# Kernel optimization log

Hardware: AMD Instinct MI355X
Metric: run time of the kernel (lower is better)

## Reference

```python
import jax, jax.numpy as jnp
import numpy as np

VOCAB, EMBED, HIDDEN, CLASSES = 32000, 256, 512, 4
BATCH, SEQ = 64, 512


def setup_inputs() -> dict:
    key = jax.random.key(0)
    ks = jax.random.split(key, 12)
    gd = EMBED + HIDDEN
    s_g = 1.0 / np.sqrt(gd)
    s_f = 1.0 / np.sqrt(HIDDEN)
    return {
        "input_ids": jax.random.randint(ks[0], (BATCH, SEQ), 0, VOCAB, dtype=jnp.int32),
        "embedding": jax.random.normal(ks[1], (VOCAB, EMBED), dtype=jnp.float32),
        "W_f": jax.random.uniform(ks[2], (HIDDEN, gd), jnp.float32, -s_g, s_g),
        "b_f": jax.random.uniform(ks[3], (HIDDEN,), jnp.float32, -s_g, s_g),
        "W_i": jax.random.uniform(ks[4], (HIDDEN, gd), jnp.float32, -s_g, s_g),
        "b_i": jax.random.uniform(ks[5], (HIDDEN,), jnp.float32, -s_g, s_g),
        "W_o": jax.random.uniform(ks[6], (HIDDEN, gd), jnp.float32, -s_g, s_g),
        "b_o": jax.random.uniform(ks[7], (HIDDEN,), jnp.float32, -s_g, s_g),
        "W_c": jax.random.uniform(ks[8], (HIDDEN, gd), jnp.float32, -s_g, s_g),
        "b_c": jax.random.uniform(ks[9], (HIDDEN,), jnp.float32, -s_g, s_g),
        "fc_w": jax.random.uniform(ks[10], (CLASSES, HIDDEN), jnp.float32, -s_f, s_f),
        "fc_b": jax.random.uniform(ks[11], (CLASSES,), jnp.float32, -s_f, s_f),
    }


def reference(input_ids, embedding, W_f, b_f, W_i, b_i, W_o, b_o, W_c, b_c, fc_w, fc_b):
    x = embedding[input_ids]                      # [B, T, E]
    B = x.shape[0]
    xs = jnp.swapaxes(x, 0, 1)                    # [T, B, E]

    def step(carry, x_t):
        h, c = carry
        inp = jnp.concatenate([h, x_t], axis=1)   # [B, H+E]
        f = jax.nn.sigmoid(inp @ W_f.T + b_f)
        i = jax.nn.sigmoid(inp @ W_i.T + b_i)
        o = jax.nn.sigmoid(inp @ W_o.T + b_o)
        g = jnp.tanh(inp @ W_c.T + b_c)
        c_new = f * c + i * g
        h_new = o * jnp.tanh(c_new)
        return (h_new, c_new), h_new

    h0 = jnp.zeros((B, HIDDEN), dtype=x.dtype)
    c0 = jnp.zeros((B, HIDDEN), dtype=x.dtype)
    _, hids = jax.lax.scan(step, (h0, c0), xs)    # hids: [T, B, H]
    max_hids = jnp.max(hids, axis=0)              # [B, H]
    logits = max_hids @ fc_w.T + fc_b             # [B, C]
    return logits
```

## Files before the change

kernel.cpp:

```cpp
#include <hip/hip_runtime.h>
#include <math.h>


#define BATCH   64
#define SEQ     512
#define EMBED   256
#define HIDDEN  512
#define GD      768
#define CLASSES 4

#define NBLK    256
#define NTHR    512
#define GROUPS  4
#define GB      64
#define CPG     16
#define UPB     8
#define ROWS    32

#define SHS  520
#define SXS  264
#define PRS  68

typedef unsigned long long __attribute__((may_alias)) ull_a;

union F2U { float f[2]; unsigned long long u; };

__device__ __forceinline__ float dpp8_sum(float v) {
  int x;
  x = __builtin_amdgcn_update_dpp(0, __float_as_int(v), 0x141, 0xF, 0xF, false);
  v += __int_as_float(x);
  x = __builtin_amdgcn_update_dpp(0, __float_as_int(v), 0x4E,  0xF, 0xF, false);
  v += __int_as_float(x);
  x = __builtin_amdgcn_update_dpp(0, __float_as_int(v), 0xB1,  0xF, 0xF, false);
  v += __int_as_float(x);
  return v;
}

__global__ __launch_bounds__(NTHR) void lstm_persistent(
    const int*   __restrict__ ids,
    const float* __restrict__ emb,
    const float* __restrict__ Wf, const float* __restrict__ bf,
    const float* __restrict__ Wi, const float* __restrict__ bi,
    const float* __restrict__ Wo, const float* __restrict__ bo,
    const float* __restrict__ Wc, const float* __restrict__ bc,
    const float* __restrict__ fcw,
    const float* __restrict__ fcb,
    float* __restrict__ out,
    float* __restrict__ ws)
{
  __shared__ __align__(16) float sH[CPG * SHS];
  __shared__ __align__(16) float sX[CPG * SXS];
  __shared__ __align__(16) float sPart[64 * PRS];
  __shared__ float sG[ROWS][CPG];
  __shared__ float sC[UPB][CPG];
  __shared__ float sM[UPB][CPG];
  __shared__ float sB[ROWS];

  const int tid = threadIdx.x;
  const int bid = blockIdx.x;
  const int g   = bid & 3;
  const int j   = bid >> 2;
  const int u0  = j * UPB;

  float*    hbufF   = ws;
  ull_a*    hbufU   = (ull_a*)ws;
  float*    wmaxF   = ws + (size_t)2 * BATCH * HIDDEN;
  ull_a*    wmaxU   = (ull_a*)wmaxF;
  unsigned* flags   = (unsigned*)(ws + (size_t)3 * BATCH * HIDDEN);
  unsigned* myflag  = flags + (g * 64 + j) * 16;

  const int sl = tid & 7;
  const int wv = tid >> 6;
  const int s  = sl + wv * 8;
  const int rg = (tid >> 3) & 7;

  float4 wh[4][2], wx4[4];
  {
    const float* Wg = (rg < 2) ? Wf : (rg < 4) ? Wi : (rg < 6) ? Wo : Wc;
    const int ub = u0 + (rg & 1) * 4;
    #pragma unroll
    for (int ri = 0; ri < 4; ++ri) {
      const float* row = Wg + (size_t)(ub + ri) * GD;
      wh[ri][0] = *(const float4*)(row + s * 8);
      wh[ri][1] = *(const float4*)(row + s * 8 + 4);
      wx4[ri]   = *(const float4*)(row + HIDDEN + s * 4);
    }
  }
  if (tid < ROWS) {
    const float* bv = (tid < 8) ? bf : (tid < 16) ? bi : (tid < 24) ? bo : bc;
    sB[tid] = bv[u0 + (tid & 7)];
  }
  if (tid < UPB * CPG) {
    ((float*)sC)[tid] = 0.0f;
    ((float*)sM)[tid] = -3.402823e38f;
  }

  const int stg_c = tid >> 5;
  const int stg_s = tid & 31;
  const int bStg  = g * CPG + stg_c;

  const float* pH = sH + s * 8;
  const float* pX = sX + s * 4;

  float4 rx0, rx1;
  {
    int id0 = ids[(size_t)bStg * SEQ];
    const float4* xs = (const float4*)(emb + (size_t)id0 * EMBED);
    rx0 = xs[stg_s * 2];
    rx1 = xs[stg_s * 2 + 1];
  }

  for (int t = 0; t < SEQ; ++t) {
    const int pb = t & 1;

    {
      float* dx = sX + stg_c * SXS + stg_s * 8;
      *(float4*)dx = rx0;
      *(float4*)(dx + 4) = rx1;
    }

    if (tid < 64) {
      const unsigned* pf = flags + (g * 64 + tid) * 16;
      while (true) {
        unsigned v = __hip_atomic_load(pf, __ATOMIC_RELAXED,
                                       __HIP_MEMORY_SCOPE_AGENT);
        if (__all((int)(v >= (unsigned)t))) break;
        __builtin_amdgcn_s_sleep(1);
      }
    }
    __atomic_signal_fence(__ATOMIC_ACQUIRE);
    __syncthreads();

    {
      const ull_a* hs = hbufU + ((size_t)pb * BATCH + bStg) * (HIDDEN / 2);
      float* dh = sH + stg_c * SHS;
      #pragma unroll
      for (int kk = 0; kk < 8; ++kk) {
        unsigned long long v = __hip_atomic_load(hs + stg_s + kk * 32,
                                                 __ATOMIC_RELAXED,
                                                 __HIP_MEMORY_SCOPE_AGENT);
        *(ull_a*)(dh + 2 * stg_s + 64 * kk) = v;
      }
    }
    __syncthreads();

    #pragma unroll
    for (int ci = 0; ci < 16; ++ci) {
      float4 xv = *(const float4*)(pX + ci * SXS);
      float4 h0 = *(const float4*)(pH + ci * SHS);
      float4 h1 = *(const float4*)(pH + ci * SHS + 4);
      float a[4];
      #pragma unroll
      for (int ri = 0; ri < 4; ++ri) {
        float t0;
        t0 = wx4[ri].x * xv.x;
        t0 = fmaf(wx4[ri].y, xv.y, t0);
        t0 = fmaf(wx4[ri].z, xv.z, t0);
        t0 = fmaf(wx4[ri].w, xv.w, t0);
        t0 = fmaf(wh[ri][0].x, h0.x, t0);
        t0 = fmaf(wh[ri][0].y, h0.y, t0);
        t0 = fmaf(wh[ri][0].z, h0.z, t0);
        t0 = fmaf(wh[ri][0].w, h0.w, t0);
        t0 = fmaf(wh[ri][1].x, h1.x, t0);
        t0 = fmaf(wh[ri][1].y, h1.y, t0);
        t0 = fmaf(wh[ri][1].z, h1.z, t0);
        t0 = fmaf(wh[ri][1].w, h1.w, t0);
        a[ri] = dpp8_sum(t0);
      }
      if ((tid & 7) == 0) {
        float* dst = sPart + (tid >> 3) * PRS + ci;
        dst[0]  = a[0];
        dst[16] = a[1];
        dst[32] = a[2];
        dst[48] = a[3];
      }
    }

    {
      const int tn = (t + 1 < SEQ) ? t + 1 : SEQ - 1;
      int idn = ids[(size_t)bStg * SEQ + tn];
      const float4* xs = (const float4*)(emb + (size_t)idn * EMBED);
      rx0 = xs[stg_s * 2];
      rx1 = xs[stg_s * 2 + 1];
    }
    __syncthreads();

    {
      const int rr  = tid >> 4;
      const int ci2 = tid & 15;
      const int rg2 = rr >> 2;
      const int idx = (rr & 3) * 16 + ci2;
      float ssum = sB[rr];
      #pragma unroll
      for (int w = 0; w < 8; ++w)
        ssum += sPart[(w * 8 + rg2) * PRS + idx];
      sG[rr][ci2] = (rr < 24) ? 1.0f / (1.0f + expf(-ssum)) : tanhf(ssum);
    }
    __syncthreads();

    if (tid < 128) {
      const int u = tid & 7, ch = tid >> 3;
      float f  = sG[u][ch];
      float i_ = sG[8 + u][ch];
      float o  = sG[16 + u][ch];
      float gg = sG[24 + u][ch];
      float cn = f * sC[u][ch] + i_ * gg;
      float h  = o * tanhf(cn);
      sC[u][ch] = cn;
      sM[u][ch] = fmaxf(sM[u][ch], h);
      __hip_atomic_store(
          hbufF + ((size_t)(pb ^ 1) * BATCH + g * CPG + ch) * HIDDEN + u0 + u,
          h, __ATOMIC_RELAXED, __HIP_MEMORY_SCOPE_AGENT);
    }
    __syncthreads();

    if (tid == 0)
      __hip_atomic_store(myflag, (unsigned)(t + 1), __ATOMIC_RELAXED,
                         __HIP_MEMORY_SCOPE_AGENT);
  }

  if (tid < 128) {
    const int u = tid & 7, ch = tid >> 3;
    __hip_atomic_store(wmaxF + (size_t)(g * CPG + ch) * HIDDEN + u0 + u,
                       sM[u][ch], __ATOMIC_RELAXED, __HIP_MEMORY_SCOPE_AGENT);
  }
  __syncthreads();
  if (tid == 0)
    __hip_atomic_store(myflag, (unsigned)(SEQ + 1), __ATOMIC_RELAXED,
                       __HIP_MEMORY_SCOPE_AGENT);

  if (j == 0) {
    if (tid < 64) {
      const unsigned* pf = flags + (g * 64 + tid) * 16;
      while (true) {
        unsigned v = __hip_atomic_load(pf, __ATOMIC_RELAXED,
                                       __HIP_MEMORY_SCOPE_AGENT);
        if (__all((int)(v >= (unsigned)(SEQ + 1)))) break;
        __builtin_amdgcn_s_sleep(1);
      }
    }
    __atomic_signal_fence(__ATOMIC_ACQUIRE);
    __syncthreads();

    const int ch = tid & 15, cls = (tid >> 4) & 3, us = tid >> 6;
    const ull_a* mrow = wmaxU + (size_t)(g * CPG + ch) * (HIDDEN / 2) + us * 32;
    const float* wrow = fcw + (size_t)cls * HIDDEN + us * 64;
    float sacc = 0.0f;
    for (int q = 0; q < 32; ++q) {
      F2U v;
      v.u = __hip_atomic_load(mrow + q, __ATOMIC_RELAXED,
                              __HIP_MEMORY_SCOPE_AGENT);
      sacc = fmaf(v.f[0], wrow[2 * q], sacc);
      sacc = fmaf(v.f[1], wrow[2 * q + 1], sacc);
    }
    float* red2 = &sG[0][0];
    red2[tid] = sacc;
    __syncthreads();
    if (tid < 64) {
      float tot = fcb[(tid >> 4) & 3];
      #pragma unroll
      for (int q = 0; q < 8; ++q) tot += red2[q * 64 + tid];
      out[(g * CPG + (tid & 15)) * CLASSES + ((tid >> 4) & 3)] = tot;
    }
  }
}

extern "C" void kernel_launch(void* const* d_in, const int* in_sizes, int n_in,
                              void* d_out, int out_size, void* d_ws, size_t ws_size,
                              hipStream_t stream) {
  const int*   ids = (const int*)  d_in[0];
  const float* emb = (const float*)d_in[1];
  const float* Wf  = (const float*)d_in[2];
  const float* bf  = (const float*)d_in[3];
  const float* Wi  = (const float*)d_in[4];
  const float* bi  = (const float*)d_in[5];
  const float* Wo  = (const float*)d_in[6];
  const float* bo  = (const float*)d_in[7];
  const float* Wc  = (const float*)d_in[8];
  const float* bc  = (const float*)d_in[9];
  const float* fcw = (const float*)d_in[10];
  const float* fcb = (const float*)d_in[11];

  hipMemsetAsync(d_ws, 0, (size_t)BATCH * HIDDEN * sizeof(float), stream);
  hipMemsetAsync((char*)d_ws + (size_t)3 * BATCH * HIDDEN * sizeof(float),
                 0, 16384, stream);

  lstm_persistent<<<dim3(NBLK), dim3(NTHR), 0, stream>>>(
      ids, emb, Wf, bf, Wi, bi, Wo, bo, Wc, bc, fcw, fcb,
      (float*)d_out, (float*)d_ws);
}
```

Before: 3.773 ms.

## Precompute x-projection before flag wait and fuse gate activation with cell update

The input-embedding part of the gate dot products for half the columns is computed before spinning on the inter-block step flags, so that work overlaps the wait for the previous hidden state. The gate reduction, activation and cell update are merged into one phase: all threads split the partial sums, combine them with DPP quad reductions, and broadcast the gates within each quad, which removes one __syncthreads per step. Staging of the next x into shared memory moves to the end of the step. The change adds 32 accumulator registers per thread, which may affect occupancy or cause spilling.

```diff
diff --git a/kernel.cpp b/kernel.cpp
--- a/kernel.cpp
+++ b/kernel.cpp
@@ -34,6 +34,12 @@
   x = __builtin_amdgcn_update_dpp(0, __float_as_int(v), 0xB1,  0xF, 0xF, false);
   v += __int_as_float(x);
   return v;
+}
+
+template <int CTRL>
+__device__ __forceinline__ float quad_bcast(float v) {
+  return __int_as_float(
+      __builtin_amdgcn_update_dpp(0, __float_as_int(v), CTRL, 0xF, 0xF, false));
 }
 
 __global__ __launch_bounds__(NTHR) void lstm_persistent(
@@ -108,15 +114,28 @@
     const float4* xs = (const float4*)(emb + (size_t)id0 * EMBED);
     rx0 = xs[stg_s * 2];
     rx1 = xs[stg_s * 2 + 1];
-  }
+    float* dx = sX + stg_c * SXS + stg_s * 8;
+    *(float4*)dx = rx0;
+    *(float4*)(dx + 4) = rx1;
+  }
+  __syncthreads();
 
   for (int t = 0; t < SEQ; ++t) {
     const int pb = t & 1;
 
-    {
-      float* dx = sX + stg_c * SXS + stg_s * 8;
-      *(float4*)dx = rx0;
-      *(float4*)(dx + 4) = rx1;
+    float accA[4][8];
+    #pragma unroll
+    for (int c8 = 0; c8 < 8; ++c8) {
+      float4 xv = *(const float4*)(pX + (c8 + 8) * SXS);
+      #pragma unroll
+      for (int ri = 0; ri < 4; ++ri) {
+        float t0;
+        t0 = wx4[ri].x * xv.x;
+        t0 = fmaf(wx4[ri].y, xv.y, t0);
+        t0 = fmaf(wx4[ri].z, xv.z, t0);
+        t0 = fmaf(wx4[ri].w, xv.w, t0);
+        accA[ri][c8] = t0;
+      }
     }
 
     if (tid < 64) {
@@ -145,7 +164,7 @@
     __syncthreads();
 
     #pragma unroll
-    for (int ci = 0; ci < 16; ++ci) {
+    for (int ci = 0; ci < 8; ++ci) {
       float4 xv = *(const float4*)(pX + ci * SXS);
       float4 h0 = *(const float4*)(pH + ci * SHS);
       float4 h1 = *(const float4*)(pH + ci * SHS + 4);
@@ -175,6 +194,33 @@
         dst[48] = a[3];
       }
     }
+    #pragma unroll
+    for (int c8 = 0; c8 < 8; ++c8) {
+      const int ci = c8 + 8;
+      float4 h0 = *(const float4*)(pH + ci * SHS);
+      float4 h1 = *(const float4*)(pH + ci * SHS + 4);
+      float a[4];
+      #pragma unroll
+      for (int ri = 0; ri < 4; ++ri) {
+        float t0 = accA[ri][c8];
+        t0 = fmaf(wh[ri][0].x, h0.x, t0);
+        t0 = fmaf(wh[ri][0].y, h0.y, t0);
+        t0 = fmaf(wh[ri][0].z, h0.z, t0);
+        t0 = fmaf(wh[ri][0].w, h0.w, t0);
+        t0 = fmaf(wh[ri][1].x, h1.x, t0);
+        t0 = fmaf(wh[ri][1].y, h1.y, t0);
+        t0 = fmaf(wh[ri][1].z, h1.z, t0);
+        t0 = fmaf(wh[ri][1].w, h1.w, t0);
+        a[ri] = dpp8_sum(t0);
+      }
+      if ((tid & 7) == 0) {
+        float* dst = sPart + (tid >> 3) * PRS + ci;
+        dst[0]  = a[0];
+        dst[16] = a[1];
+        dst[32] = a[2];
+        dst[48] = a[3];
+      }
+    }
 
     {
       const int tn = (t + 1 < SEQ) ? t + 1 : SEQ - 1;
@@ -186,31 +232,49 @@
     __syncthreads();
 
     {
-      const int rr  = tid >> 4;
-      const int ci2 = tid & 15;
-      const int rg2 = rr >> 2;
-      const int idx = (rr & 3) * 16 + ci2;
-      float ssum = sB[rr];
-      #pragma unroll
-      for (int w = 0; w < 8; ++w)
-        ssum += sPart[(w * 8 + rg2) * PRS + idx];
-      sG[rr][ci2] = (rr < 24) ? 1.0f / (1.0f + expf(-ssum)) : tanhf(ssum);
-    }
-    __syncthreads();
-
-    if (tid < 128) {
-      const int u = tid & 7, ch = tid >> 3;
-      float f  = sG[u][ch];
-      float i_ = sG[8 + u][ch];
-      float o  = sG[16 + u][ch];
-      float gg = sG[24 + u][ch];
-      float cn = f * sC[u][ch] + i_ * gg;
+      const int q  = tid & 3;
+      const int qi = tid >> 2;
+      const int u  = qi & 7, ch = qi >> 3;
+      float s4[4];
+      #pragma unroll
+      for (int gi = 0; gi < 4; ++gi) {
+        const int rr  = gi * 8 + u;
+        const int rg2 = rr >> 2;
+        const int idxp = (rr & 3) * 16 + ch;
+        float p = sPart[((2 * q) * 8 + rg2) * PRS + idxp]
+                + sPart[((2 * q + 1) * 8 + rg2) * PRS + idxp];
+        s4[gi] = p;
+      }
+      #pragma unroll
+      for (int gi = 0; gi < 4; ++gi) {
+        int x;
+        x = __builtin_amdgcn_update_dpp(0, __float_as_int(s4[gi]), 0xB1, 0xF, 0xF, false);
+        s4[gi] += __int_as_float(x);
+        x = __builtin_amdgcn_update_dpp(0, __float_as_int(s4[gi]), 0x4E, 0xF, 0xF, false);
+        s4[gi] += __int_as_float(x);
+      }
+      float v = (q == 0) ? s4[0] : (q == 1) ? s4[1] : (q == 2) ? s4[2] : s4[3];
+      v += sB[q * 8 + u];
+      float y;
+      if (q < 3) y = 1.0f / (1.0f + expf(-v));
+      else       y = tanhf(v);
+      float f  = quad_bcast<0x00>(y);
+      float i_ = quad_bcast<0x55>(y);
+      float o  = quad_bcast<0xAA>(y);
+      float gg = quad_bcast<0xFF>(y);
+      float cc = sC[u][ch];
+      float cn = f * cc + i_ * gg;
       float h  = o * tanhf(cn);
-      sC[u][ch] = cn;
-      sM[u][ch] = fmaxf(sM[u][ch], h);
-      __hip_atomic_store(
-          hbufF + ((size_t)(pb ^ 1) * BATCH + g * CPG + ch) * HIDDEN + u0 + u,
-          h, __ATOMIC_RELAXED, __HIP_MEMORY_SCOPE_AGENT);
+      if (q == 0) {
+        sC[u][ch] = cn;
+        sM[u][ch] = fmaxf(sM[u][ch], h);
+        __hip_atomic_store(
+            hbufF + ((size_t)(pb ^ 1) * BATCH + g * CPG + ch) * HIDDEN + u0 + u,
+            h, __ATOMIC_RELAXED, __HIP_MEMORY_SCOPE_AGENT);
+      }
+      float* dx = sX + stg_c * SXS + stg_s * 8;
+      *(float4*)dx = rx0;
+      *(float4*)(dx + 4) = rx1;
     }
     __syncthreads();
 
@@ -246,12 +310,12 @@
     const ull_a* mrow = wmaxU + (size_t)(g * CPG + ch) * (HIDDEN / 2) + us * 32;
     const float* wrow = fcw + (size_t)cls * HIDDEN + us * 64;
     float sacc = 0.0f;
-    for (int q = 0; q < 32; ++q) {
+    for (int q2 = 0; q2 < 32; ++q2) {
       F2U v;
-      v.u = __hip_atomic_load(mrow + q, __ATOMIC_RELAXED,
+      v.u = __hip_atomic_load(mrow + q2, __ATOMIC_RELAXED,
                               __HIP_MEMORY_SCOPE_AGENT);
-      sacc = fmaf(v.f[0], wrow[2 * q], sacc);
-      sacc = fmaf(v.f[1], wrow[2 * q + 1], sacc);
+      sacc = fmaf(v.f[0], wrow[2 * q2], sacc);
+      sacc = fmaf(v.f[1], wrow[2 * q2 + 1], sacc);
     }
     float* red2 = &sG[0][0];
     red2[tid] = sacc;
@@ -259,7 +323,7 @@
     if (tid < 64) {
       float tot = fcb[(tid >> 4) & 3];
       #pragma unroll
-      for (int q = 0; q < 8; ++q) tot += red2[q * 64 + tid];
+      for (int q2 = 0; q2 < 8; ++q2) tot += red2[q2 * 64 + tid];
       out[(g * CPG + (tid & 15)) * CLASSES + ((tid >> 4) & 3)] = tot;
     }
   }
```

New measurement: 4.384 ms. +16.2%, slower.
